# Performance work log

Measured on AMD Instinct MI355X. Metric: run time of the kernel, lower is better.

## Reference

```python
import jax, jax.numpy as jnp
import numpy as np

B = 1048576
EPS = 1e-5

def _lin_params(key, din, dout):
    k1, k2 = jax.random.split(key)
    bound = 1.0 / np.sqrt(din)
    w = jax.random.uniform(k1, (din, dout), minval=-bound, maxval=bound, dtype=jnp.float32)
    b = jax.random.uniform(k2, (dout,), minval=-bound, maxval=bound, dtype=jnp.float32)
    return w, b

def setup_inputs() -> dict:
    key = jax.random.key(0)
    ks = jax.random.split(key, 10)
    x = jax.random.normal(ks[0], (B, 8), dtype=jnp.float32)
    dims = [(8, 16), (16, 16), (16, 12), (12, 8), (8, 4), (4, 4), (4, 4), (4, 1)]
    names = ['fm', 'c1', 'p1', 'c2', 'p2', 'c3', 'r', 'h']
    inp = {'x': x,
           'bn_g': jnp.ones((8,), jnp.float32),
           'bn_b': jnp.zeros((8,), jnp.float32)}
    for i, (nm, (di, do)) in enumerate(zip(names, dims)):
        w, b = _lin_params(ks[i + 1], di, do)
        inp['w_' + nm] = w
        inp['b_' + nm] = b
    return inp

def reference(x, bn_g, bn_b, w_fm, b_fm, w_c1, b_c1, w_p1, b_p1, w_c2, b_c2,
              w_p2, b_p2, w_c3, b_c3, w_r, b_r, w_h, b_h):
    # BatchNorm1d (training mode): batch statistics, biased variance
    mu = jnp.mean(x, axis=0)
    var = jnp.mean((x - mu) ** 2, axis=0)
    h = (x - mu) * jax.lax.rsqrt(var + EPS) * bn_g + bn_b
    h = jnp.tanh(h @ w_fm + b_fm)   # [B,16] feature_map
    h = jnp.tanh(h @ w_c1 + b_c1)   # [B,16] conv1
    h = jnp.tanh(h @ w_p1 + b_p1)   # [B,12] pool1
    h = jnp.tanh(h @ w_c2 + b_c2)   # [B,8]  conv2
    h = jnp.tanh(h @ w_p2 + b_p2)   # [B,4]  pool2
    h = jnp.tanh(h @ w_c3 + b_c3)   # [B,4]  conv3
    res = jax.nn.relu(h @ w_r + b_r)  # [B,4] residual branch
    h = h + res
    return jax.nn.sigmoid(h @ w_h + b_h)  # [B,1]
```

## Files before the change

### kernel.cpp

```cpp
#include <hip/hip_runtime.h>

#define B_ROWS 1048576
#define NTHREADS2 (B_ROWS / 2)

__device__ __forceinline__ float fast_tanh(float x) {
    float e = __builtin_amdgcn_exp2f(x * 2.8853900817779268f);
    return 1.0f - 2.0f * __builtin_amdgcn_rcpf(e + 1.0f);
}

__device__ __forceinline__ float fast_sigmoid(float x) {
    float e = __builtin_amdgcn_exp2f(x * -1.4426950408889634f);
    return __builtin_amdgcn_rcpf(1.0f + e);
}

__global__ __launch_bounds__(256) void bn_stats(const float* __restrict__ x,
                                                float* __restrict__ ws) {
    const int tid = blockIdx.x * 256 + threadIdx.x;
    float s[8], q[8];
#pragma unroll
    for (int c = 0; c < 8; ++c) { s[c] = 0.f; q[c] = 0.f; }
    const float4* x4 = (const float4*)x;
#pragma unroll 4
    for (int k = 0; k < 16; ++k) {
        int r = tid + k * 65536;
        float4 a = x4[2 * r];
        float4 b = x4[2 * r + 1];
        s[0] += a.x; s[1] += a.y; s[2] += a.z; s[3] += a.w;
        s[4] += b.x; s[5] += b.y; s[6] += b.z; s[7] += b.w;
        q[0] += a.x * a.x; q[1] += a.y * a.y; q[2] += a.z * a.z; q[3] += a.w * a.w;
        q[4] += b.x * b.x; q[5] += b.y * b.y; q[6] += b.z * b.z; q[7] += b.w * b.w;
    }
#pragma unroll
    for (int off = 32; off > 0; off >>= 1) {
#pragma unroll
        for (int c = 0; c < 8; ++c) {
            s[c] += __shfl_down(s[c], off);
            q[c] += __shfl_down(q[c], off);
        }
    }
    __shared__ float red[4][16];
    const int lane = threadIdx.x & 63;
    const int wave = threadIdx.x >> 6;
    if (lane == 0) {
#pragma unroll
        for (int c = 0; c < 8; ++c) { red[wave][c] = s[c]; red[wave][8 + c] = q[c]; }
    }
    __syncthreads();
    if (threadIdx.x < 16) {
        float acc = red[0][threadIdx.x] + red[1][threadIdx.x] +
                    red[2][threadIdx.x] + red[3][threadIdx.x];
        atomicAdd(&ws[threadIdx.x], acc);
    }
}

template<int DIN, int DOUT>
__device__ __forceinline__ void linear2(const float* __restrict__ a, const float* __restrict__ b,
                                        float* __restrict__ oa, float* __restrict__ ob,
                                        const float* __restrict__ w, const float* __restrict__ bias) {
#pragma unroll
    for (int j = 0; j < DOUT; ++j) { float t = bias[j]; oa[j] = t; ob[j] = t; }
#pragma unroll
    for (int i = 0; i < DIN; ++i) {
        float ai = a[i], bi = b[i];
#pragma unroll
        for (int j = 0; j < DOUT; ++j) {
            float ww = w[i * DOUT + j];
            oa[j] = fmaf(ai, ww, oa[j]);
            ob[j] = fmaf(bi, ww, ob[j]);
        }
    }
}

template<int N>
__device__ __forceinline__ void tanh2(float* a, float* b) {
#pragma unroll
    for (int j = 0; j < N; ++j) { a[j] = fast_tanh(a[j]); b[j] = fast_tanh(b[j]); }
}

__global__ __launch_bounds__(256) void qcnn_main(
    const float* __restrict__ x,
    const float* __restrict__ bn_g, const float* __restrict__ bn_b,
    const float* __restrict__ w_fm, const float* __restrict__ b_fm,
    const float* __restrict__ w_c1, const float* __restrict__ b_c1,
    const float* __restrict__ w_p1, const float* __restrict__ b_p1,
    const float* __restrict__ w_c2, const float* __restrict__ b_c2,
    const float* __restrict__ w_p2, const float* __restrict__ b_p2,
    const float* __restrict__ w_c3, const float* __restrict__ b_c3,
    const float* __restrict__ w_r,  const float* __restrict__ b_r,
    const float* __restrict__ w_h,  const float* __restrict__ b_h,
    const float* __restrict__ ws, float* __restrict__ out)
{
    const float invB = 1.0f / (float)B_ROWS;
    float scale[8], shift[8];
#pragma unroll
    for (int c = 0; c < 8; ++c) {
        float mu  = ws[c] * invB;
        float var = fmaf(-mu, mu, ws[8 + c] * invB);
        float sc  = bn_g[c] * rsqrtf(var + 1e-5f);
        scale[c] = sc;
        shift[c] = fmaf(-mu, sc, bn_b[c]);
    }

    const int tid = blockIdx.x * 256 + threadIdx.x;
    const int r0 = tid, r1 = tid + NTHREADS2;
    const float4* x4 = (const float4*)x;
    float4 xa0 = x4[2 * r0], xa1 = x4[2 * r0 + 1];
    float4 xb0 = x4[2 * r1], xb1 = x4[2 * r1 + 1];

    float a8[8], b8[8];
    a8[0] = xa0.x; a8[1] = xa0.y; a8[2] = xa0.z; a8[3] = xa0.w;
    a8[4] = xa1.x; a8[5] = xa1.y; a8[6] = xa1.z; a8[7] = xa1.w;
    b8[0] = xb0.x; b8[1] = xb0.y; b8[2] = xb0.z; b8[3] = xb0.w;
    b8[4] = xb1.x; b8[5] = xb1.y; b8[6] = xb1.z; b8[7] = xb1.w;
#pragma unroll
    for (int c = 0; c < 8; ++c) {
        a8[c] = fmaf(a8[c], scale[c], shift[c]);
        b8[c] = fmaf(b8[c], scale[c], shift[c]);
    }

    float a16[16], b16[16];
    linear2<8, 16>(a8, b8, a16, b16, w_fm, b_fm);  tanh2<16>(a16, b16);
    float t16a[16], t16b[16];
    linear2<16, 16>(a16, b16, t16a, t16b, w_c1, b_c1);  tanh2<16>(t16a, t16b);
    float a12[12], b12[12];
    linear2<16, 12>(t16a, t16b, a12, b12, w_p1, b_p1);  tanh2<12>(a12, b12);
    float c8a[8], c8b[8];
    linear2<12, 8>(a12, b12, c8a, c8b, w_c2, b_c2);  tanh2<8>(c8a, c8b);
    float a4[4], b4[4];
    linear2<8, 4>(c8a, c8b, a4, b4, w_p2, b_p2);  tanh2<4>(a4, b4);
    float c4a[4], c4b[4];
    linear2<4, 4>(a4, b4, c4a, c4b, w_c3, b_c3);  tanh2<4>(c4a, c4b);
    float r4a[4], r4b[4];
    linear2<4, 4>(c4a, c4b, r4a, r4b, w_r, b_r);
#pragma unroll
    for (int j = 0; j < 4; ++j) {
        c4a[j] += fmaxf(r4a[j], 0.f);
        c4b[j] += fmaxf(r4b[j], 0.f);
    }
    float oa[1], ob[1];
    linear2<4, 1>(c4a, c4b, oa, ob, w_h, b_h);
    out[r0] = fast_sigmoid(oa[0]);
    out[r1] = fast_sigmoid(ob[0]);
}

extern "C" void kernel_launch(void* const* d_in, const int* in_sizes, int n_in,
                              void* d_out, int out_size, void* d_ws, size_t ws_size,
                              hipStream_t stream) {
    const float* x    = (const float*)d_in[0];
    const float* bn_g = (const float*)d_in[1];
    const float* bn_b = (const float*)d_in[2];
    const float* w_fm = (const float*)d_in[3];
    const float* b_fm = (const float*)d_in[4];
    const float* w_c1 = (const float*)d_in[5];
    const float* b_c1 = (const float*)d_in[6];
    const float* w_p1 = (const float*)d_in[7];
    const float* b_p1 = (const float*)d_in[8];
    const float* w_c2 = (const float*)d_in[9];
    const float* b_c2 = (const float*)d_in[10];
    const float* w_p2 = (const float*)d_in[11];
    const float* b_p2 = (const float*)d_in[12];
    const float* w_c3 = (const float*)d_in[13];
    const float* b_c3 = (const float*)d_in[14];
    const float* w_r  = (const float*)d_in[15];
    const float* b_r  = (const float*)d_in[16];
    const float* w_h  = (const float*)d_in[17];
    const float* b_h  = (const float*)d_in[18];
    float* out = (float*)d_out;
    float* ws  = (float*)d_ws;

    (void)hipMemsetAsync(d_ws, 0, 16 * sizeof(float), stream);
    bn_stats<<<256, 256, 0, stream>>>(x, ws);
    qcnn_main<<<B_ROWS / 512, 256, 0, stream>>>(
        x, bn_g, bn_b, w_fm, b_fm, w_c1, b_c1, w_p1, b_p1, w_c2, b_c2,
        w_p2, b_p2, w_c3, b_c3, w_r, b_r, w_h, b_h, ws, out);
}
```

Before: 151.2 us.

## Fold batchnorm into first layer and compute MLP with packed fp16 dot2

A new single-block prep kernel folds the batchnorm scale and shift into the first layer's weights and bias, then packs all weights as fp16 pairs in the workspace. The main kernel converts activations to packed half2 and uses fdot2 instructions with fp32 accumulation, processing one row per thread with twice as many blocks. The stats kernel switches to 1024 blocks with fewer iterations each. This cuts ALU work per row and removes the per-thread BN setup, at the cost of an extra launch and fp16 rounding of activations and weights, which may hurt accuracy.

```diff
diff --git a/kernel.cpp b/kernel.cpp
--- a/kernel.cpp
+++ b/kernel.cpp
@@ -1,7 +1,28 @@
 #include <hip/hip_runtime.h>
+#include <stdint.h>
 
 #define B_ROWS 1048576
-#define NTHREADS2 (B_ROWS / 2)
+
+typedef __fp16 h2 __attribute__((ext_vector_type(2)));
+
+#define WPK_OFF 16
+#define BIA_OFF 386
+#define W_FM 0
+#define W_C1 64
+#define W_P1 192
+#define W_C2 288
+#define W_P2 336
+#define W_C3 352
+#define W_R  360
+#define W_H  368
+#define B_FM 0
+#define B_C1 16
+#define B_P1 32
+#define B_C2 44
+#define B_P2 52
+#define B_C3 56
+#define B_R  60
+#define B_H  64
 
 __device__ __forceinline__ float fast_tanh(float x) {
     float e = __builtin_amdgcn_exp2f(x * 2.8853900817779268f);
@@ -20,9 +41,9 @@
 #pragma unroll
     for (int c = 0; c < 8; ++c) { s[c] = 0.f; q[c] = 0.f; }
     const float4* x4 = (const float4*)x;
-#pragma unroll 4
-    for (int k = 0; k < 16; ++k) {
-        int r = tid + k * 65536;
+#pragma unroll
+    for (int k = 0; k < 4; ++k) {
+        int r = tid + k * 262144;
         float4 a = x4[2 * r];
         float4 b = x4[2 * r + 1];
         s[0] += a.x; s[1] += a.y; s[2] += a.z; s[3] += a.w;
@@ -54,31 +75,29 @@
 }
 
 template<int DIN, int DOUT>
-__device__ __forceinline__ void linear2(const float* __restrict__ a, const float* __restrict__ b,
-                                        float* __restrict__ oa, float* __restrict__ ob,
-                                        const float* __restrict__ w, const float* __restrict__ bias) {
-#pragma unroll
-    for (int j = 0; j < DOUT; ++j) { float t = bias[j]; oa[j] = t; ob[j] = t; }
-#pragma unroll
-    for (int i = 0; i < DIN; ++i) {
-        float ai = a[i], bi = b[i];
-#pragma unroll
-        for (int j = 0; j < DOUT; ++j) {
-            float ww = w[i * DOUT + j];
-            oa[j] = fmaf(ai, ww, oa[j]);
-            ob[j] = fmaf(bi, ww, ob[j]);
+__device__ void pack_layer(const float* __restrict__ w, const float* __restrict__ b,
+                           uint32_t* __restrict__ wdst, float* __restrict__ bdst,
+                           const float* sc, const float* sh, bool fold) {
+    for (int idx = threadIdx.x; idx < DOUT * (DIN / 2); idx += blockDim.x) {
+        int j = idx / (DIN / 2), i2 = idx % (DIN / 2);
+        float w0 = w[(2 * i2) * DOUT + j];
+        float w1 = w[(2 * i2 + 1) * DOUT + j];
+        if (fold) { w0 *= sc[2 * i2]; w1 *= sc[2 * i2 + 1]; }
+        h2 h; h.x = (__fp16)w0; h.y = (__fp16)w1;
+        wdst[j * (DIN / 2) + i2] = __builtin_bit_cast(uint32_t, h);
+    }
+    for (int j = threadIdx.x; j < DOUT; j += blockDim.x) {
+        float bb = b[j];
+        if (fold) {
+#pragma unroll
+            for (int i = 0; i < 8; ++i) bb += sh[i] * w[i * DOUT + j];
         }
-    }
-}
-
-template<int N>
-__device__ __forceinline__ void tanh2(float* a, float* b) {
-#pragma unroll
-    for (int j = 0; j < N; ++j) { a[j] = fast_tanh(a[j]); b[j] = fast_tanh(b[j]); }
-}
-
-__global__ __launch_bounds__(256) void qcnn_main(
-    const float* __restrict__ x,
+        bdst[j] = bb;
+    }
+}
+
+__global__ __launch_bounds__(256) void prep(
+    float* __restrict__ ws,
     const float* __restrict__ bn_g, const float* __restrict__ bn_b,
     const float* __restrict__ w_fm, const float* __restrict__ b_fm,
     const float* __restrict__ w_c1, const float* __restrict__ b_c1,
@@ -87,60 +106,100 @@
     const float* __restrict__ w_p2, const float* __restrict__ b_p2,
     const float* __restrict__ w_c3, const float* __restrict__ b_c3,
     const float* __restrict__ w_r,  const float* __restrict__ b_r,
-    const float* __restrict__ w_h,  const float* __restrict__ b_h,
-    const float* __restrict__ ws, float* __restrict__ out)
+    const float* __restrict__ w_h,  const float* __restrict__ b_h)
 {
     const float invB = 1.0f / (float)B_ROWS;
-    float scale[8], shift[8];
+    float sc[8], sh[8];
 #pragma unroll
     for (int c = 0; c < 8; ++c) {
         float mu  = ws[c] * invB;
         float var = fmaf(-mu, mu, ws[8 + c] * invB);
-        float sc  = bn_g[c] * rsqrtf(var + 1e-5f);
-        scale[c] = sc;
-        shift[c] = fmaf(-mu, sc, bn_b[c]);
-    }
+        float s   = bn_g[c] * rsqrtf(var + 1e-5f);
+        sc[c] = s;
+        sh[c] = fmaf(-mu, s, bn_b[c]);
+    }
+    uint32_t* wpk = (uint32_t*)(ws + WPK_OFF);
+    float*    bpk = ws + BIA_OFF;
+    pack_layer<8, 16>(w_fm, b_fm, wpk + W_FM, bpk + B_FM, sc, sh, true);
+    pack_layer<16,16>(w_c1, b_c1, wpk + W_C1, bpk + B_C1, sc, sh, false);
+    pack_layer<16,12>(w_p1, b_p1, wpk + W_P1, bpk + B_P1, sc, sh, false);
+    pack_layer<12, 8>(w_c2, b_c2, wpk + W_C2, bpk + B_C2, sc, sh, false);
+    pack_layer<8,  4>(w_p2, b_p2, wpk + W_P2, bpk + B_P2, sc, sh, false);
+    pack_layer<4,  4>(w_c3, b_c3, wpk + W_C3, bpk + B_C3, sc, sh, false);
+    pack_layer<4,  4>(w_r,  b_r,  wpk + W_R,  bpk + B_R,  sc, sh, false);
+    pack_layer<4,  1>(w_h,  b_h,  wpk + W_H,  bpk + B_H,  sc, sh, false);
+}
+
+template<int DIN, int DOUT>
+__device__ __forceinline__ void layer_dot(const h2* __restrict__ apk, float* __restrict__ out,
+                                          const uint32_t* __restrict__ wpk,
+                                          const float* __restrict__ bias) {
+#pragma unroll
+    for (int j = 0; j < DOUT; ++j) {
+        float acc = bias[j];
+#pragma unroll
+        for (int i2 = 0; i2 < DIN / 2; ++i2) {
+            h2 w = __builtin_bit_cast(h2, wpk[j * (DIN / 2) + i2]);
+            acc = __builtin_amdgcn_fdot2(apk[i2], w, acc, false);
+        }
+        out[j] = acc;
+    }
+}
+
+template<int N>
+__device__ __forceinline__ void tanh_pack(const float* __restrict__ in, h2* __restrict__ apk) {
+#pragma unroll
+    for (int k = 0; k < N / 2; ++k) {
+        float t0 = fast_tanh(in[2 * k]);
+        float t1 = fast_tanh(in[2 * k + 1]);
+        apk[k] = __builtin_amdgcn_cvt_pkrtz(t0, t1);
+    }
+}
+
+__global__ __launch_bounds__(256) void qcnn_main(
+    const float* __restrict__ x,
+    const float* __restrict__ ws, float* __restrict__ out)
+{
+    const uint32_t* wpk = (const uint32_t*)(ws + WPK_OFF);
+    const float*    bpk = ws + BIA_OFF;
 
     const int tid = blockIdx.x * 256 + threadIdx.x;
-    const int r0 = tid, r1 = tid + NTHREADS2;
     const float4* x4 = (const float4*)x;
-    float4 xa0 = x4[2 * r0], xa1 = x4[2 * r0 + 1];
-    float4 xb0 = x4[2 * r1], xb1 = x4[2 * r1 + 1];
-
-    float a8[8], b8[8];
-    a8[0] = xa0.x; a8[1] = xa0.y; a8[2] = xa0.z; a8[3] = xa0.w;
-    a8[4] = xa1.x; a8[5] = xa1.y; a8[6] = xa1.z; a8[7] = xa1.w;
-    b8[0] = xb0.x; b8[1] = xb0.y; b8[2] = xb0.z; b8[3] = xb0.w;
-    b8[4] = xb1.x; b8[5] = xb1.y; b8[6] = xb1.z; b8[7] = xb1.w;
-#pragma unroll
-    for (int c = 0; c < 8; ++c) {
-        a8[c] = fmaf(a8[c], scale[c], shift[c]);
-        b8[c] = fmaf(b8[c], scale[c], shift[c]);
-    }
-
-    float a16[16], b16[16];
-    linear2<8, 16>(a8, b8, a16, b16, w_fm, b_fm);  tanh2<16>(a16, b16);
-    float t16a[16], t16b[16];
-    linear2<16, 16>(a16, b16, t16a, t16b, w_c1, b_c1);  tanh2<16>(t16a, t16b);
-    float a12[12], b12[12];
-    linear2<16, 12>(t16a, t16b, a12, b12, w_p1, b_p1);  tanh2<12>(a12, b12);
-    float c8a[8], c8b[8];
-    linear2<12, 8>(a12, b12, c8a, c8b, w_c2, b_c2);  tanh2<8>(c8a, c8b);
-    float a4[4], b4[4];
-    linear2<8, 4>(c8a, c8b, a4, b4, w_p2, b_p2);  tanh2<4>(a4, b4);
-    float c4a[4], c4b[4];
-    linear2<4, 4>(a4, b4, c4a, c4b, w_c3, b_c3);  tanh2<4>(c4a, c4b);
-    float r4a[4], r4b[4];
-    linear2<4, 4>(c4a, c4b, r4a, r4b, w_r, b_r);
-#pragma unroll
-    for (int j = 0; j < 4; ++j) {
-        c4a[j] += fmaxf(r4a[j], 0.f);
-        c4b[j] += fmaxf(r4b[j], 0.f);
-    }
-    float oa[1], ob[1];
-    linear2<4, 1>(c4a, c4b, oa, ob, w_h, b_h);
-    out[r0] = fast_sigmoid(oa[0]);
-    out[r1] = fast_sigmoid(ob[0]);
+    float4 xa = x4[2 * tid], xb = x4[2 * tid + 1];
+
+    h2 a8[4];
+    a8[0] = __builtin_amdgcn_cvt_pkrtz(xa.x, xa.y);
+    a8[1] = __builtin_amdgcn_cvt_pkrtz(xa.z, xa.w);
+    a8[2] = __builtin_amdgcn_cvt_pkrtz(xb.x, xb.y);
+    a8[3] = __builtin_amdgcn_cvt_pkrtz(xb.z, xb.w);
+
+    float o16[16]; h2 p16[8];
+    layer_dot<8, 16>(a8, o16, wpk + W_FM, bpk + B_FM);  tanh_pack<16>(o16, p16);
+    float o16b[16]; h2 p16b[8];
+    layer_dot<16,16>(p16, o16b, wpk + W_C1, bpk + B_C1); tanh_pack<16>(o16b, p16b);
+    float o12[12]; h2 p12[6];
+    layer_dot<16,12>(p16b, o12, wpk + W_P1, bpk + B_P1); tanh_pack<12>(o12, p12);
+    float o8[8]; h2 p8[4];
+    layer_dot<12, 8>(p12, o8, wpk + W_C2, bpk + B_C2);   tanh_pack<8>(o8, p8);
+    float o4[4]; h2 p4[2];
+    layer_dot<8,  4>(p8, o4, wpk + W_P2, bpk + B_P2);    tanh_pack<4>(o4, p4);
+    float c4[4];
+    layer_dot<4,  4>(p4, c4, wpk + W_C3, bpk + B_C3);
+#pragma unroll
+    for (int j = 0; j < 4; ++j) c4[j] = fast_tanh(c4[j]);
+    h2 pc4[2];
+    pc4[0] = __builtin_amdgcn_cvt_pkrtz(c4[0], c4[1]);
+    pc4[1] = __builtin_amdgcn_cvt_pkrtz(c4[2], c4[3]);
+    float r4[4];
+    layer_dot<4,  4>(pc4, r4, wpk + W_R, bpk + B_R);
+#pragma unroll
+    for (int j = 0; j < 4; ++j) c4[j] += fmaxf(r4[j], 0.f);
+    h2 ph[2];
+    ph[0] = __builtin_amdgcn_cvt_pkrtz(c4[0], c4[1]);
+    ph[1] = __builtin_amdgcn_cvt_pkrtz(c4[2], c4[3]);
+    float oh[1];
+    layer_dot<4,  1>(ph, oh, wpk + W_H, bpk + B_H);
+    out[tid] = fast_sigmoid(oh[0]);
 }
 
 extern "C" void kernel_launch(void* const* d_in, const int* in_sizes, int n_in,
@@ -169,8 +228,8 @@
     float* ws  = (float*)d_ws;
 
     (void)hipMemsetAsync(d_ws, 0, 16 * sizeof(float), stream);
-    bn_stats<<<256, 256, 0, stream>>>(x, ws);
-    qcnn_main<<<B_ROWS / 512, 256, 0, stream>>>(
-        x, bn_g, bn_b, w_fm, b_fm, w_c1, b_c1, w_p1, b_p1, w_c2, b_c2,
-        w_p2, b_p2, w_c3, b_c3, w_r, b_r, w_h, b_h, ws, out);
-}
+    bn_stats<<<1024, 256, 0, stream>>>(x, ws);
+    prep<<<1, 256, 0, stream>>>(ws, bn_g, bn_b, w_fm, b_fm, w_c1, b_c1, w_p1, b_p1,
+                                w_c2, b_c2, w_p2, b_p2, w_c3, b_c3, w_r, b_r, w_h, b_h);
+    qcnn_main<<<B_ROWS / 256, 256, 0, stream>>>(x, ws, out);
+}
```

New measurement: 155.3 us. 1.03x slower.
